# Kernel tuning notes

Hardware: AMD Instinct MI355X
Metric: run time of the kernel (lower is better)

Reference implementation:

```python
import jax, jax.numpy as jnp
import numpy as np

DIM = 1024
HEADS = 16
DHEAD = 64
INNER = HEADS * DHEAD
EPS = 1e-5


def layer_norm(x, g, b):
    mu = jnp.mean(x, axis=-1, keepdims=True)
    var = jnp.mean(jnp.square(x - mu), axis=-1, keepdims=True)
    return (x - mu) * jax.lax.rsqrt(var + EPS) * g + b


def apply_rope(x, cos, sin):
    # x: [b, h, s, d]; cos/sin broadcast as [1, 1, s, d/2]
    d2 = x.shape[-1] // 2
    x1, x2 = x[..., :d2], x[..., d2:]
    return jnp.concatenate([x1 * cos - x2 * sin, x2 * cos + x1 * sin], axis=-1)


def setup_inputs() -> dict:
    key = jax.random.key(0)
    ks = jax.random.split(key, 10)
    B, N, S = 8, 256, 4096
    latents = jax.random.normal(ks[0], (B, N, DIM), dtype=jnp.float32)
    context = jax.random.normal(ks[1], (B, S, DIM), dtype=jnp.float32)
    cos = jax.random.uniform(ks[2], (S, DHEAD // 2), dtype=jnp.float32)
    sin = jax.random.uniform(ks[3], (S, DHEAD // 2), dtype=jnp.float32)
    init = lambda k, shp, fan_in: jax.random.normal(k, shp, dtype=jnp.float32) / np.sqrt(fan_in)
    return {
        "latents": latents,
        "context": context,
        "cos": cos,
        "sin": sin,
        "ln_lat_g": jnp.ones((DIM,), jnp.float32),
        "ln_lat_b": jnp.zeros((DIM,), jnp.float32),
        "ln_ctx_g": jnp.ones((DIM,), jnp.float32),
        "ln_ctx_b": jnp.zeros((DIM,), jnp.float32),
        "Wq": init(ks[4], (DIM, INNER), DIM),
        "Wkv": init(ks[5], (DIM, 2 * INNER), DIM),
        "Wo": init(ks[6], (INNER, DIM), INNER),
        "bo": jnp.zeros((DIM,), jnp.float32),
    }


def reference(latents, context, cos, sin, ln_lat_g, ln_lat_b, ln_ctx_g, ln_ctx_b, Wq, Wkv, Wo, bo):
    b, n, _ = latents.shape
    s = context.shape[1]
    lat = layer_norm(latents, ln_lat_g, ln_lat_b)
    ctx = layer_norm(context, ln_ctx_g, ln_ctx_b)
    q = (lat @ Wq).reshape(b, n, HEADS, DHEAD).transpose(0, 2, 1, 3)   # [b,h,n,d]
    kv = ctx @ Wkv
    k, v = jnp.split(kv, 2, axis=-1)
    k = k.reshape(b, s, HEADS, DHEAD).transpose(0, 2, 1, 3)           # [b,h,s,d]
    v = v.reshape(b, s, HEADS, DHEAD).transpose(0, 2, 1, 3)
    k = apply_rope(k, cos[None, None], sin[None, None])
    scale = DHEAD ** (-0.5)
    attn = jnp.einsum('bhnd,bhsd->bhns', q, k) * scale
    attn = jnp.clip(attn, -11.0, 11.0)
    attn = jax.nn.softmax(attn, axis=-1)
    out = jnp.einsum('bhns,bhsd->bhnd', attn, v)
    out = out.transpose(0, 2, 1, 3).reshape(b, n, INNER)
    return out @ Wo + bo
```

## Files before the change

### kernel.cpp

```cpp
#include <hip/hip_runtime.h>
#include <hip/hip_bf16.h>
#include <math.h>

#define DIM   1024
#define HEADS 16
#define DHEAD 64
#define NB    8
#define NLAT  256
#define SCTX  4096

typedef short bf16x8 __attribute__((ext_vector_type(8)));
typedef float f32x4  __attribute__((ext_vector_type(4)));

__device__ __forceinline__ unsigned short f2b(float f) {
    union { float f; unsigned u; } x; x.f = f;
    unsigned r = x.u + 0x7FFFu + ((x.u >> 16) & 1u);
    return (unsigned short)(r >> 16);
}

__device__ __forceinline__ unsigned pkbf16(float a, float b) {
    float2 f2; f2.x = a; f2.y = b;
    __hip_bfloat162 h = __float22bfloat162_rn(f2);
    union { __hip_bfloat162 h; unsigned u; } cv; cv.h = h;
    return cv.u;
}

#define LN_WBLOCKS ((NB * NLAT + NB * SCTX) / 4)
__global__ __launch_bounds__(256) void prep_all(
    const float* __restrict__ latents, const float* __restrict__ context,
    const float* __restrict__ g_lat, const float* __restrict__ b_lat,
    const float* __restrict__ g_ctx, const float* __restrict__ b_ctx,
    const float* __restrict__ Wq, const float* __restrict__ Wkv,
    const float* __restrict__ Wo,
    unsigned short* __restrict__ lat_b, unsigned short* __restrict__ ctx_b,
    unsigned short* __restrict__ Wqb, unsigned short* __restrict__ Wkvb,
    unsigned short* __restrict__ Wob)
{
    int gb = blockIdx.x, t = threadIdx.x;
    if (gb < LN_WBLOCKS) {
        int wid = t >> 6, lane = t & 63;
        int row = gb * 4 + wid;
        const float* x; const float* g; const float* b; unsigned short* y; int r;
        if (row < NB * NLAT) { x = latents; g = g_lat; b = b_lat; y = lat_b; r = row; }
        else { x = context; g = g_ctx; b = b_ctx; y = ctx_b; r = row - NB * NLAT; }
        const float4* xr = (const float4*)(x + (size_t)r * DIM);
        float4 v[4];
        float s = 0.f, sq = 0.f;
        #pragma unroll
        for (int i = 0; i < 4; ++i) {
            v[i] = xr[lane + i * 64];
            s  += v[i].x + v[i].y + v[i].z + v[i].w;
            sq += v[i].x * v[i].x + v[i].y * v[i].y + v[i].z * v[i].z + v[i].w * v[i].w;
        }
        #pragma unroll
        for (int off = 32; off > 0; off >>= 1) {
            s  += __shfl_xor(s, off);
            sq += __shfl_xor(sq, off);
        }
        float mu = s * (1.0f / DIM);
        float rs = rsqrtf(sq * (1.0f / DIM) - mu * mu + 1e-5f);
        #pragma unroll
        for (int i = 0; i < 4; ++i) {
            float4 gg = ((const float4*)g)[lane + i * 64];
            float4 bb = ((const float4*)b)[lane + i * 64];
            ushort4 o;
            o.x = f2b((v[i].x - mu) * rs * gg.x + bb.x);
            o.y = f2b((v[i].y - mu) * rs * gg.y + bb.y);
            o.z = f2b((v[i].z - mu) * rs * gg.z + bb.z);
            o.w = f2b((v[i].w - mu) * rs * gg.w + bb.w);
            ((ushort4*)(y + (size_t)r * DIM))[lane + i * 64] = o;
        }
    } else {
        __shared__ unsigned short tile[32][33];
        int id = gb - LN_WBLOCKS;
        int z = id >> 10, y = (id >> 5) & 31, xb = id & 31;
        const float* W; unsigned short* Wt; int N, coloff = 0;
        switch (z) {
            case 0: W = Wq;  Wt = Wqb;  N = DIM;     break;
            case 1: W = Wkv; Wt = Wkvb; N = 2 * DIM; break;
            case 2: W = Wkv; Wt = Wkvb; N = 2 * DIM; coloff = DIM; break;
            default: W = Wo; Wt = Wob;  N = DIM;     break;
        }
        int n0 = xb * 32 + coloff, k0 = y * 32;
        int tx = t & 31, ty = t >> 5;
        #pragma unroll
        for (int i = 0; i < 4; ++i) {
            int k = k0 + ty + i * 8;
            tile[tx][ty + i * 8] = f2b(W[(size_t)k * N + n0 + tx]);
        }
        __syncthreads();
        #pragma unroll
        for (int i = 0; i < 4; ++i) {
            int n = n0 + ty + i * 8;
            Wt[(size_t)n * DIM + k0 + tx] = tile[ty + i * 8][tx];
        }
    }
}

__global__ __launch_bounds__(256, 2) void gemm_mfma(
    const unsigned short* __restrict__ A, const unsigned short* __restrict__ Bn,
    const unsigned short* __restrict__ Aq, const unsigned short* __restrict__ Bq,
    int K, const float* __restrict__ bias,
    const float* __restrict__ cosp, const float* __restrict__ sinp,
    float* __restrict__ outf,
    unsigned short* __restrict__ outk, unsigned short* __restrict__ outv,
    unsigned short* __restrict__ outq,
    int mode, int ldc)
{
    __shared__ __align__(16) unsigned short As[128 * 64];
    __shared__ __align__(16) unsigned short Bs[128 * 64];
    int t = threadIdx.x;
    int wave = t >> 6, lane = t & 63;
    int g = blockIdx.x;
    int m_tile, n_tile;
    if (mode == 2) {
        if (g >= 4096) {
            g -= 4096; mode = 1;
            A = Aq; Bn = Bq;
            n_tile = g & 7; m_tile = g >> 3;
        } else {
            int xcd = g & 7, j = g >> 3;
            n_tile = j & 15;
            m_tile = (xcd << 5) + (j >> 4);
        }
    } else {
        n_tile = g & 7; m_tile = g >> 3;
    }
    int m_base = m_tile * 128, n_base = n_tile * 128;
    int wr = wave >> 1, wc = wave & 1;
    int quad = lane >> 4, ln = lane & 15;

    f32x4 zero = {0.f, 0.f, 0.f, 0.f};
    f32x4 acc[4][4];
    #pragma unroll
    for (int i = 0; i < 4; ++i)
        #pragma unroll
        for (int j = 0; j < 4; ++j) acc[i][j] = zero;

    const unsigned short* Ag = A  + (size_t)m_base * K;
    const unsigned short* Bg = Bn + (size_t)n_base * K;

    int srow  = lane >> 3;
    int schk  = ((lane & 7) ^ srow) * 8;

    for (int k0 = 0; k0 < K; k0 += 64) {
        __syncthreads();
        #pragma unroll
        for (int j = 0; j < 4; ++j) {
            int grp = j * 4 + wave;
            int row = grp * 8 + srow;
            __builtin_amdgcn_global_load_lds(
                (const __attribute__((address_space(1))) void*)(Ag + (size_t)row * K + k0 + schk),
                (__attribute__((address_space(3))) void*)(As + grp * 512 + lane * 8),
                16, 0, 0);
            __builtin_amdgcn_global_load_lds(
                (const __attribute__((address_space(1))) void*)(Bg + (size_t)row * K + k0 + schk),
                (__attribute__((address_space(3))) void*)(Bs + grp * 512 + lane * 8),
                16, 0, 0);
        }
        __syncthreads();
        #pragma unroll
        for (int kk = 0; kk < 2; ++kk) {
            bf16x8 af[4], bfr[4];
            int slot = ((kk * 4 + quad) ^ (ln & 7)) * 8;
            #pragma unroll
            for (int i = 0; i < 4; ++i) {
                af[i]  = *(const bf16x8*)(As + (wr * 64 + i * 16 + ln) * 64 + slot);
                bfr[i] = *(const bf16x8*)(Bs + (wc * 64 + i * 16 + ln) * 64 + slot);
            }
            #pragma unroll
            for (int i = 0; i < 4; ++i)
                #pragma unroll
                for (int j = 0; j < 4; ++j)
                    acc[i][j] = __builtin_amdgcn_mfma_f32_16x16x32_bf16(af[i], bfr[j], acc[i][j], 0, 0, 0);
        }
    }

    int cl = ln, rq = quad;
    if (mode == 2 && n_base >= DIM) {
        #pragma unroll
        for (int i = 0; i < 4; ++i) {
            int s0 = m_base + wr * 64 + i * 16 + rq * 4;
            int b  = s0 >> 12, s = s0 & 4095;
            #pragma unroll
            for (int j = 0; j < 4; ++j) {
                int n2 = n_base + wc * 64 + j * 16 + cl - DIM;
                int h = n2 >> 6, d = n2 & 63;
                ushort4 pk;
                pk.x = f2b(acc[i][j][0]); pk.y = f2b(acc[i][j][1]);
                pk.z = f2b(acc[i][j][2]); pk.w = f2b(acc[i][j][3]);
                *(ushort4*)(outv + (((size_t)(b * HEADS + h) * DHEAD + d) * SCTX) + s) = pk;
            }
        }
    } else if (mode == 2) {
        #pragma unroll
        for (int i = 0; i < 4; ++i) {
            #pragma unroll
            for (int r = 0; r < 4; ++r) {
                int m = m_base + wr * 64 + i * 16 + rq * 4 + r;
                int b = m >> 12, s = m & 4095;
                #pragma unroll
                for (int j = 0; j < 2; ++j) {
                    int n = n_base + wc * 64 + j * 16 + cl;
                    int h = n >> 6, d1 = n & 63;
                    float x1 = acc[i][j][r], x2 = acc[i][j + 2][r];
                    float c  = cosp[s * 32 + d1];
                    float sn = sinp[s * 32 + d1];
                    unsigned short* kr =
                        outk + (((size_t)(b * HEADS + h) * SCTX + s) * DHEAD) + d1;
                    kr[0]  = f2b(x1 * c - x2 * sn);
                    kr[32] = f2b(x2 * c + x1 * sn);
                }
            }
        }
    } else {
        #pragma unroll
        for (int i = 0; i < 4; ++i) {
            #pragma unroll
            for (int j = 0; j < 4; ++j) {
                #pragma unroll
                for (int r = 0; r < 4; ++r) {
                    int m = m_base + wr * 64 + i * 16 + rq * 4 + r;
                    int n = n_base + wc * 64 + j * 16 + cl;
                    float cv = acc[i][j][r];
                    if (mode == 0) {
                        outf[(size_t)m * ldc + n] = cv + bias[n];
                    } else {
                        int b = m >> 8, nn = m & 255;
                        int h = n >> 6, d = n & 63;
                        outq[(((size_t)(b * HEADS + h) * NLAT + nn) * DHEAD) + d] =
                            f2b(cv * 0.18033688f);
                    }
                }
            }
        }
    }
}

#define PPAD 72
#define CLIP2 15.8696454f

__global__ __launch_bounds__(256, 3) void attn_mfma(
    const unsigned short* __restrict__ qb,
    const unsigned short* __restrict__ kb,
    const unsigned short* __restrict__ vtb,
    float* __restrict__ accp,
    float* __restrict__ lp)
{
    __shared__ __align__(16) unsigned short Ks[2][64 * 64];
    __shared__ __align__(16) unsigned short Vs[2][64 * 64];
    __shared__ __align__(16) unsigned short Ps[4 * 32 * PPAD];

    int t = threadIdx.x, w = t >> 6, l = t & 63;
    int bx = blockIdx.x;
    int g  = ((bx >> 4) << 3) + (bx & 7);
    int qh = (bx >> 3) & 1;
    int bh = g >> 2;
    int sh = g & 3;
    int quad = l >> 4, ln = l & 15;
    int q0 = qh * 128 + w * 32;

    bf16x8 qf[2][2];
    const unsigned short* qbase = qb + ((size_t)bh * NLAT + q0) * DHEAD;
    #pragma unroll
    for (int qsub = 0; qsub < 2; ++qsub)
        #pragma unroll
        for (int kc = 0; kc < 2; ++kc)
            qf[qsub][kc] = *(const bf16x8*)(qbase + (qsub * 16 + ln) * DHEAD + kc * 32 + quad * 8);

    f32x4 acc[2][4];
    #pragma unroll
    for (int i = 0; i < 2; ++i)
        #pragma unroll
        for (int j = 0; j < 4; ++j) acc[i][j] = (f32x4){0.f, 0.f, 0.f, 0.f};
    float lacc[2] = {0.f, 0.f};

    int srow = t >> 3;
    int schk = t & 7;
    int cpos = schk ^ (srow & 7);
    const unsigned short* kgb = kb  + (size_t)bh * SCTX * DHEAD;
    const unsigned short* vgb = vtb + (size_t)bh * DHEAD * SCTX;
    unsigned short* Pw = Ps + w * 32 * PPAD;

    const int s_begin = sh * 1024;
    const int NT = 1024 / 64;

    uint4 kreg[2], vreg[2];
    #pragma unroll
    for (int i = 0; i < 2; ++i) {
        int row = srow + 32 * i;
        kreg[i] = *(const uint4*)(kgb + (size_t)(s_begin + row) * DHEAD + schk * 8);
        vreg[i] = *(const uint4*)(vgb + (size_t)row * SCTX + s_begin + schk * 8);
    }
    #pragma unroll
    for (int i = 0; i < 2; ++i) {
        int row = srow + 32 * i;
        *(uint4*)(&Ks[0][row * 64 + cpos * 8]) = kreg[i];
        *(uint4*)(&Vs[0][row * 64 + cpos * 8]) = vreg[i];
    }

    for (int it = 0; it < NT; ++it) {
        int buf = it & 1;
        if (it + 1 < NT) {
            int s0n = s_begin + (it + 1) * 64;
            #pragma unroll
            for (int i = 0; i < 2; ++i) {
                int row = srow + 32 * i;
                kreg[i] = *(const uint4*)(kgb + (size_t)(s0n + row) * DHEAD + schk * 8);
                vreg[i] = *(const uint4*)(vgb + (size_t)row * SCTX + s0n + schk * 8);
            }
        }
        __syncthreads();

        #pragma unroll
        for (int msub = 0; msub < 4; ++msub) {
            bf16x8 af[2];
            #pragma unroll
            for (int kc = 0; kc < 2; ++kc) {
                int sr = msub * 16 + ln;
                int ck = (4 * kc + quad) ^ (ln & 7);
                af[kc] = *(const bf16x8*)(&Ks[buf][sr * 64 + ck * 8]);
            }
            #pragma unroll
            for (int nsub = 0; nsub < 2; ++nsub) {
                f32x4 c = {0.f, 0.f, 0.f, 0.f};
                c = __builtin_amdgcn_mfma_f32_16x16x32_bf16(af[0], qf[nsub][0], c, 0, 0, 0);
                c = __builtin_amdgcn_mfma_f32_16x16x32_bf16(af[1], qf[nsub][1], c, 0, 0, 0);
                float p[4];
                #pragma unroll
                for (int r = 0; r < 4; ++r) {
                    float sc = __builtin_amdgcn_fmed3f(c[r], -CLIP2, CLIP2);
                    p[r] = __builtin_amdgcn_exp2f(sc - CLIP2);
                    lacc[nsub] += p[r];
                }
                uint2 pk;
                pk.x = pkbf16(p[0], p[1]);
                pk.y = pkbf16(p[2], p[3]);
                *(uint2*)(Pw + (nsub * 16 + ln) * PPAD + msub * 16 + quad * 4) = pk;
            }
        }
        #pragma unroll
        for (int kc = 0; kc < 2; ++kc) {
            bf16x8 pa[2];
            #pragma unroll
            for (int qsub = 0; qsub < 2; ++qsub)
                pa[qsub] = *(const bf16x8*)(Pw + (qsub * 16 + ln) * PPAD + kc * 32 + quad * 8);
            #pragma unroll
            for (int dsub = 0; dsub < 4; ++dsub) {
                int dr = dsub * 16 + ln;
                int ck = (4 * kc + quad) ^ (ln & 7);
                bf16x8 vb = *(const bf16x8*)(&Vs[buf][dr * 64 + ck * 8]);
                acc[0][dsub] = __builtin_amdgcn_mfma_f32_16x16x32_bf16(pa[0], vb, acc[0][dsub], 0, 0, 0);
                acc[1][dsub] = __builtin_amdgcn_mfma_f32_16x16x32_bf16(pa[1], vb, acc[1][dsub], 0, 0, 0);
            }
        }
        if (it + 1 < NT) {
            #pragma unroll
            for (int i = 0; i < 2; ++i) {
                int row = srow + 32 * i;
                *(uint4*)(&Ks[buf ^ 1][row * 64 + cpos * 8]) = kreg[i];
                *(uint4*)(&Vs[buf ^ 1][row * 64 + cpos * 8]) = vreg[i];
            }
        }
    }

    float* accs = accp + (size_t)sh * (NB * HEADS * NLAT * DHEAD);
    float* ls   = lp   + (size_t)sh * (NB * HEADS * NLAT);

    #pragma unroll
    for (int nsub = 0; nsub < 2; ++nsub) {
        float v = lacc[nsub];
        v += __shfl_xor(v, 16);
        v += __shfl_xor(v, 32);
        if (l < 16)
            ls[bh * NLAT + q0 + nsub * 16 + l] = v;
    }
    #pragma unroll
    for (int qsub = 0; qsub < 2; ++qsub)
        #pragma unroll
        for (int dsub = 0; dsub < 4; ++dsub)
            #pragma unroll
            for (int r = 0; r < 4; ++r) {
                int qg = q0 + qsub * 16 + quad * 4 + r;
                int dg = dsub * 16 + ln;
                accs[((size_t)bh * NLAT + qg) * DHEAD + dg] = acc[qsub][dsub][r];
            }
}

__global__ __launch_bounds__(256) void attn_finalize(
    const float* __restrict__ accp, const float* __restrict__ lp,
    unsigned short* __restrict__ aob)
{
    const int ACC = NB * HEADS * NLAT * DHEAD;
    const int LSZ = NB * HEADS * NLAT;
    int idx = blockIdx.x * 256 + threadIdx.x;
    int d = idx & 63;
    int rest = idx >> 6;
    int n = rest & 255, bh = rest >> 8;
    int b = bh >> 4, h = bh & 15;
    float a = accp[idx] + accp[idx + ACC] + accp[idx + 2 * ACC] + accp[idx + 3 * ACC];
    float l = lp[rest] + lp[rest + LSZ] + lp[rest + 2 * LSZ] + lp[rest + 3 * LSZ];
    aob[(((size_t)b * NLAT + n) * HEADS + h) * DHEAD + d] = f2b(a / l);
}

extern "C" void kernel_launch(void* const* d_in, const int* in_sizes, int n_in,
                              void* d_out, int out_size, void* d_ws, size_t ws_size,
                              hipStream_t stream) {
    const float* latents  = (const float*)d_in[0];
    const float* context  = (const float*)d_in[1];
    const float* cosp     = (const float*)d_in[2];
    const float* sinp     = (const float*)d_in[3];
    const float* ln_lat_g = (const float*)d_in[4];
    const float* ln_lat_b = (const float*)d_in[5];
    const float* ln_ctx_g = (const float*)d_in[6];
    const float* ln_ctx_b = (const float*)d_in[7];
    const float* Wq  = (const float*)d_in[8];
    const float* Wkv = (const float*)d_in[9];
    const float* Wo  = (const float*)d_in[10];
    const float* bo  = (const float*)d_in[11];
    float* out = (float*)d_out;

    char* base = (char*)d_ws;
    unsigned short* lat_b = (unsigned short*)(base + 0);
    unsigned short* ctx_b = (unsigned short*)(base + 4194304);
    unsigned short* Wqb   = (unsigned short*)(base + 71303168);
    unsigned short* Wkvb  = (unsigned short*)(base + 73400320);
    unsigned short* Wob   = (unsigned short*)(base + 77594624);
    unsigned short* q_b   = (unsigned short*)(base + 79691776);
    unsigned short* k_b   = (unsigned short*)(base + 83886080);
    unsigned short* vT_b  = (unsigned short*)(base + 150994944);
    float*          accp  = (float*)(base + 218103808);
    float*          lp    = (float*)(base + 251658240);
    unsigned short* aob   = (unsigned short*)(base + 252182528);

    hipLaunchKernelGGL(prep_all, dim3(LN_WBLOCKS + 4096), dim3(256), 0, stream,
                       latents, context, ln_lat_g, ln_lat_b, ln_ctx_g, ln_ctx_b,
                       Wq, Wkv, Wo, lat_b, ctx_b, Wqb, Wkvb, Wob);
    hipLaunchKernelGGL(gemm_mfma, dim3(4096 + 128), dim3(256), 0, stream,
                       ctx_b, Wkvb, lat_b, Wqb, DIM, (const float*)nullptr,
                       cosp, sinp,
                       (float*)nullptr, k_b, vT_b, q_b, 2, 0);
    hipLaunchKernelGGL(attn_mfma, dim3(NB * HEADS * 8), dim3(256), 0, stream,
                       q_b, k_b, vT_b, accp, lp);
    hipLaunchKernelGGL(attn_finalize, dim3(NB * HEADS * NLAT * DHEAD / 256), dim3(256), 0, stream,
                       accp, lp, aob);
    hipLaunchKernelGGL(gemm_mfma, dim3(128), dim3(256), 0, stream,
                       aob, Wob, (const unsigned short*)nullptr, (const unsigned short*)nullptr,
                       DIM, bo,
                       (const float*)nullptr, (const float*)nullptr,
                       out, (unsigned short*)nullptr, (unsigned short*)nullptr,
                       (unsigned short*)nullptr, 0, DIM);
}
```

Before: 524.3 us.

## Use direct global-to-LDS loads in attention and split QKV GEMM into three launches

The attention kernel now stages K and V tiles with global_load_lds instead of loading into registers and writing to shared memory. The swizzle moves to the source address, and a single barrier per iteration replaces the old one. The QKV projection GEMM is split into three launches of 1408 blocks each, using a block offset and a new tile mapping that groups N tiles in blocks of 8 per XCD. The goal is to cut register pressure and VGPR-to-LDS store traffic in attention and to improve cache locality in the GEMM, at the cost of two extra kernel launches.

```diff
diff --git a/kernel.cpp b/kernel.cpp
--- a/kernel.cpp
+++ b/kernel.cpp
@@ -112,6 +112,7 @@
     int t = threadIdx.x;
     int wave = t >> 6, lane = t & 63;
     int g = blockIdx.x;
+    if (mode == 2) g += ldc;
     int m_tile, n_tile;
     if (mode == 2) {
         if (g >= 4096) {
@@ -120,8 +121,9 @@
             n_tile = g & 7; m_tile = g >> 3;
         } else {
             int xcd = g & 7, j = g >> 3;
-            n_tile = j & 15;
-            m_tile = (xcd << 5) + (j >> 4);
+            int ngrp = j >> 8;
+            n_tile = ngrp * 8 + (j & 7);
+            m_tile = (xcd << 5) + ((j >> 3) & 31);
         }
     } else {
         n_tile = g & 7; m_tile = g >> 3;
@@ -253,10 +255,10 @@
 
     int t = threadIdx.x, w = t >> 6, l = t & 63;
     int bx = blockIdx.x;
-    int g  = ((bx >> 4) << 3) + (bx & 7);
+    int gg = ((bx >> 4) << 3) + (bx & 7);
     int qh = (bx >> 3) & 1;
-    int bh = g >> 2;
-    int sh = g & 3;
+    int bh = gg >> 2;
+    int sh = gg & 3;
     int quad = l >> 4, ln = l & 15;
     int q0 = qh * 128 + w * 32;
 
@@ -275,42 +277,39 @@
         for (int j = 0; j < 4; ++j) acc[i][j] = (f32x4){0.f, 0.f, 0.f, 0.f};
     float lacc[2] = {0.f, 0.f};
 
-    int srow = t >> 3;
-    int schk = t & 7;
-    int cpos = schk ^ (srow & 7);
     const unsigned short* kgb = kb  + (size_t)bh * SCTX * DHEAD;
     const unsigned short* vgb = vtb + (size_t)bh * DHEAD * SCTX;
     unsigned short* Pw = Ps + w * 32 * PPAD;
 
+    int srow8 = l >> 3;
+    int csrc  = (l & 7) ^ srow8;
+
+    auto STAGE = [&](int s0, int bi) {
+        #pragma unroll
+        for (int i = 0; i < 2; ++i) {
+            int rbase = w * 8 + i * 32;
+            int row = rbase + srow8;
+            __builtin_amdgcn_global_load_lds(
+                (const __attribute__((address_space(1))) void*)(kgb + (size_t)(s0 + row) * DHEAD + csrc * 8),
+                (__attribute__((address_space(3))) void*)(&Ks[bi][rbase * 64] + (size_t)l * 8),
+                16, 0, 0);
+            __builtin_amdgcn_global_load_lds(
+                (const __attribute__((address_space(1))) void*)(vgb + (size_t)row * SCTX + s0 + csrc * 8),
+                (__attribute__((address_space(3))) void*)(&Vs[bi][rbase * 64] + (size_t)l * 8),
+                16, 0, 0);
+        }
+    };
+
     const int s_begin = sh * 1024;
     const int NT = 1024 / 64;
 
-    uint4 kreg[2], vreg[2];
-    #pragma unroll
-    for (int i = 0; i < 2; ++i) {
-        int row = srow + 32 * i;
-        kreg[i] = *(const uint4*)(kgb + (size_t)(s_begin + row) * DHEAD + schk * 8);
-        vreg[i] = *(const uint4*)(vgb + (size_t)row * SCTX + s_begin + schk * 8);
-    }
-    #pragma unroll
-    for (int i = 0; i < 2; ++i) {
-        int row = srow + 32 * i;
-        *(uint4*)(&Ks[0][row * 64 + cpos * 8]) = kreg[i];
-        *(uint4*)(&Vs[0][row * 64 + cpos * 8]) = vreg[i];
-    }
+    STAGE(s_begin, 0);
+    __syncthreads();
 
     for (int it = 0; it < NT; ++it) {
         int buf = it & 1;
-        if (it + 1 < NT) {
-            int s0n = s_begin + (it + 1) * 64;
-            #pragma unroll
-            for (int i = 0; i < 2; ++i) {
-                int row = srow + 32 * i;
-                kreg[i] = *(const uint4*)(kgb + (size_t)(s0n + row) * DHEAD + schk * 8);
-                vreg[i] = *(const uint4*)(vgb + (size_t)row * SCTX + s0n + schk * 8);
-            }
-        }
-        __syncthreads();
+        if (it + 1 < NT)
+            STAGE(s_begin + (it + 1) * 64, buf ^ 1);
 
         #pragma unroll
         for (int msub = 0; msub < 4; ++msub) {
@@ -354,14 +353,7 @@
                 acc[1][dsub] = __builtin_amdgcn_mfma_f32_16x16x32_bf16(pa[1], vb, acc[1][dsub], 0, 0, 0);
             }
         }
-        if (it + 1 < NT) {
-            #pragma unroll
-            for (int i = 0; i < 2; ++i) {
-                int row = srow + 32 * i;
-                *(uint4*)(&Ks[buf ^ 1][row * 64 + cpos * 8]) = kreg[i];
-                *(uint4*)(&Vs[buf ^ 1][row * 64 + cpos * 8]) = vreg[i];
-            }
-        }
+        __syncthreads();
     }
 
     float* accs = accp + (size_t)sh * (NB * HEADS * NLAT * DHEAD);
@@ -436,10 +428,18 @@
     hipLaunchKernelGGL(prep_all, dim3(LN_WBLOCKS + 4096), dim3(256), 0, stream,
                        latents, context, ln_lat_g, ln_lat_b, ln_ctx_g, ln_ctx_b,
                        Wq, Wkv, Wo, lat_b, ctx_b, Wqb, Wkvb, Wob);
-    hipLaunchKernelGGL(gemm_mfma, dim3(4096 + 128), dim3(256), 0, stream,
+    hipLaunchKernelGGL(gemm_mfma, dim3(1408), dim3(256), 0, stream,
                        ctx_b, Wkvb, lat_b, Wqb, DIM, (const float*)nullptr,
                        cosp, sinp,
                        (float*)nullptr, k_b, vT_b, q_b, 2, 0);
+    hipLaunchKernelGGL(gemm_mfma, dim3(1408), dim3(256), 0, stream,
+                       ctx_b, Wkvb, lat_b, Wqb, DIM, (const float*)nullptr,
+                       cosp, sinp,
+                       (float*)nullptr, k_b, vT_b, q_b, 2, 1408);
+    hipLaunchKernelGGL(gemm_mfma, dim3(1408), dim3(256), 0, stream,
+                       ctx_b, Wkvb, lat_b, Wqb, DIM, (const float*)nullptr,
+                       cosp, sinp,
+                       (float*)nullptr, k_b, vT_b, q_b, 2, 2816);
     hipLaunchKernelGGL(attn_mfma, dim3(NB * HEADS * 8), dim3(256), 0, stream,
                        q_b, k_b, vT_b, accp, lp);
     hipLaunchKernelGGL(attn_finalize, dim3(NB * HEADS * NLAT * DHEAD / 256), dim3(256), 0, stream,
```

After: 507.5 us. -3.2%, faster.
